# Performance work log

Hardware: AMD Instinct MI355X
Metric: run time of the kernel (lower is better)

The kernel has to match this reference:

```python
import jax, jax.numpy as jnp
import numpy as np

N, A, B, C = 256, 1024, 64, 16


def setup_inputs() -> dict:
    key = jax.random.key(0)
    k1, k2, k3 = jax.random.split(key, 3)
    x = jax.random.normal(k1, (N, A), dtype=jnp.float32)
    weight = jax.random.normal(k2, (A, B * C), dtype=jnp.float32) * 0.02
    bias = jax.random.normal(k3, (B,), dtype=jnp.float32) * 0.02
    return {"x": x, "weight": weight, "bias": bias}


def reference(x, weight, bias):
    # x: [N, A]; weight: [A, B*C]; bias: [B]
    n = x.shape[0]
    mat = (x @ weight).reshape(n, B, C)              # [N, B, C]
    # pairwise L1 over the C (kernel) axis -> [N, N, B]
    l1 = jnp.abs(mat[:, None, :, :] - mat[None, :, :, :]).sum(axis=-1)
    # exp(-L1), sum over the first (broadcast) axis as in the torch code,
    # which includes the self term exp(0)=1
    out = jnp.exp(-l1).sum(axis=0) + bias            # [N, B]
    return out
```

## Files before the change

### kernel.cpp

```cpp
#include <hip/hip_runtime.h>

#define LOG2E 1.4426950408889634f

typedef __bf16 bf16x8 __attribute__((ext_vector_type(8)));
typedef float  f32x4  __attribute__((ext_vector_type(4)));

__device__ inline unsigned short f2bf(float f){
  unsigned u = __float_as_uint(f);
  unsigned r = u + 0x7FFFu + ((u >> 16) & 1u);
  return (unsigned short)(r >> 16);
}
__device__ inline unsigned pack2(float lo, float hi){
  return (unsigned)f2bf(lo) | ((unsigned)f2bf(hi) << 16);
}

__global__ __launch_bounds__(256) void k_gemm_ks(const float* __restrict__ X,
                                                 const float* __restrict__ Wm,
                                                 float* __restrict__ P){
  __shared__ unsigned short As[64 * 72];
  __shared__ unsigned short Bs[64 * 72];
  const int m0 = blockIdx.x * 64, n0 = blockIdx.y * 64;
  const int k0 = blockIdx.z * 256;
  const int t = threadIdx.x;
  const int lane = t & 63, w = t >> 6;
  const int wrow = (w & 1) * 32, wcol = (w >> 1) * 32;
  const int r16 = lane & 15, quad = lane >> 4;

  const int ar = t >> 2, aq = t & 3;
  const int bc = t & 15, bg = t >> 4;
  const float* ap = X + (size_t)(m0 + ar) * 1024 + k0 + aq * 16;
  const float* bp = Wm + (size_t)k0 * 1024 + n0 + bc * 4;

  f32x4 acc[2][2];
  #pragma unroll
  for (int p = 0; p < 2; ++p)
    #pragma unroll
    for (int q = 0; q < 2; ++q)
      #pragma unroll
      for (int e = 0; e < 4; ++e) acc[p][q][e] = 0.f;

  float4 pa[4], pb[4];
  #pragma unroll
  for (int r = 0; r < 4; ++r) pa[r] = *(const float4*)(ap + r * 4);
  #pragma unroll
  for (int r = 0; r < 4; ++r) pb[r] = *(const float4*)(bp + (size_t)(4 * bg + r) * 1024);

  #pragma unroll
  for (int kt = 0; kt < 256; kt += 64){
    __syncthreads();
    {
      unsigned short* d = &As[ar * 72 + aq * 16];
      uint4 o;
      o.x = pack2(pa[0].x, pa[0].y); o.y = pack2(pa[0].z, pa[0].w);
      o.z = pack2(pa[1].x, pa[1].y); o.w = pack2(pa[1].z, pa[1].w);
      *(uint4*)d = o;
      o.x = pack2(pa[2].x, pa[2].y); o.y = pack2(pa[2].z, pa[2].w);
      o.z = pack2(pa[3].x, pa[3].y); o.w = pack2(pa[3].z, pa[3].w);
      *(uint4*)(d + 8) = o;
    }
    {
      #pragma unroll
      for (int e = 0; e < 4; ++e){
        const int n = bc * 4 + e;
        uint2 o;
        o.x = pack2(((const float*)&pb[0])[e], ((const float*)&pb[1])[e]);
        o.y = pack2(((const float*)&pb[2])[e], ((const float*)&pb[3])[e]);
        const int cw = (bg >> 1) ^ ((n >> 3) & 7);
        *(uint2*)(&Bs[n * 72 + cw * 8 + (bg & 1) * 4]) = o;
      }
    }
    __syncthreads();
    if (kt < 192){
      #pragma unroll
      for (int r = 0; r < 4; ++r) pa[r] = *(const float4*)(ap + kt + 64 + r * 4);
      #pragma unroll
      for (int r = 0; r < 4; ++r) pb[r] = *(const float4*)(bp + (size_t)(kt + 64 + 4 * bg + r) * 1024);
    }
    #pragma unroll
    for (int kk = 0; kk < 2; ++kk){
      const int ko = kk * 32 + quad * 8;
      bf16x8 a0 = *(const bf16x8*)(&As[(wrow      + r16) * 72 + ko]);
      bf16x8 a1 = *(const bf16x8*)(&As[(wrow + 16 + r16) * 72 + ko]);
      const int c = kk * 4 + quad;
      const int nb0 = wcol + r16, nb1 = wcol + 16 + r16;
      bf16x8 b0 = *(const bf16x8*)(&Bs[nb0 * 72 + ((c ^ ((nb0 >> 3) & 7)) * 8)]);
      bf16x8 b1 = *(const bf16x8*)(&Bs[nb1 * 72 + ((c ^ ((nb1 >> 3) & 7)) * 8)]);
      acc[0][0] = __builtin_amdgcn_mfma_f32_16x16x32_bf16(a0, b0, acc[0][0], 0, 0, 0);
      acc[0][1] = __builtin_amdgcn_mfma_f32_16x16x32_bf16(a0, b1, acc[0][1], 0, 0, 0);
      acc[1][0] = __builtin_amdgcn_mfma_f32_16x16x32_bf16(a1, b0, acc[1][0], 0, 0, 0);
      acc[1][1] = __builtin_amdgcn_mfma_f32_16x16x32_bf16(a1, b1, acc[1][1], 0, 0, 0);
    }
  }
  float* Pz = P + (size_t)blockIdx.z * 256 * 1024;
  #pragma unroll
  for (int p = 0; p < 2; ++p)
    #pragma unroll
    for (int q = 0; q < 2; ++q)
      #pragma unroll
      for (int r = 0; r < 4; ++r){
        const int row = m0 + wrow + p * 16 + quad * 4 + r;
        const int col = n0 + wcol + q * 16 + r16;
        Pz[(size_t)row * 1024 + col] = acc[p][q][r];
      }
}

__global__ __launch_bounds__(1024) void k_pair(const float* __restrict__ P,
                                               const float* __restrict__ bias,
                                               float* __restrict__ out){
  __shared__ float L[256 * 16];
  __shared__ float red[16][64];
  const int b = blockIdx.x >> 2, jc = blockIdx.x & 3;
  const int t = threadIdx.x, lane = t & 63, w = t >> 6;

  {
    const int i = t >> 2, q = t & 3;
    const float* base = P + (size_t)i * 1024 + b * 16 + q * 4;
    float4 s0 = *(const float4*)(base);
    float4 s1 = *(const float4*)(base + 256 * 1024);
    float4 s2 = *(const float4*)(base + 512 * 1024);
    float4 s3 = *(const float4*)(base + 768 * 1024);
    float4 r;
    r.x = (s0.x + s1.x) + (s2.x + s3.x);
    r.y = (s0.y + s1.y) + (s2.y + s3.y);
    r.z = (s0.z + s1.z) + (s2.z + s3.z);
    r.w = (s0.w + s1.w) + (s2.w + s3.w);
    *(float4*)(&L[i * 16 + q * 4]) = r;
  }
  __syncthreads();

  const int j = jc * 64 + lane;
  float oj[16];
  #pragma unroll
  for (int q = 0; q < 4; ++q){
    float4 v = *(const float4*)(&L[j * 16 + q * 4]);
    oj[q*4+0] = v.x; oj[q*4+1] = v.y; oj[q*4+2] = v.z; oj[q*4+3] = v.w;
  }

  float acc = 0.f;
  const int i0 = w * 16;
  #pragma unroll 4
  for (int ii = i0; ii < i0 + 16; ++ii){
    const float4* fr = (const float4*)(&L[ii * 16]);
    float4 f0 = fr[0], f1 = fr[1], f2 = fr[2], f3 = fr[3];
    float p0 = fabsf(oj[0]  - f0.x) + fabsf(oj[1]  - f0.y)
             + fabsf(oj[2]  - f0.z) + fabsf(oj[3]  - f0.w);
    float p1 = fabsf(oj[4]  - f1.x) + fabsf(oj[5]  - f1.y)
             + fabsf(oj[6]  - f1.z) + fabsf(oj[7]  - f1.w);
    float p2 = fabsf(oj[8]  - f2.x) + fabsf(oj[9]  - f2.y)
             + fabsf(oj[10] - f2.z) + fabsf(oj[11] - f2.w);
    float p3 = fabsf(oj[12] - f3.x) + fabsf(oj[13] - f3.y)
             + fabsf(oj[14] - f3.z) + fabsf(oj[15] - f3.w);
    acc += exp2f(-LOG2E * ((p0 + p1) + (p2 + p3)));
  }
  red[w][lane] = acc;
  __syncthreads();
  if (w == 0){
    float tot = 0.f;
    #pragma unroll
    for (int ww = 0; ww < 16; ++ww) tot += red[ww][lane];
    out[(size_t)j * 64 + b] = tot + bias[b];
  }
}

extern "C" void kernel_launch(void* const* d_in, const int* in_sizes, int n_in,
                              void* d_out, int out_size, void* d_ws, size_t ws_size,
                              hipStream_t stream){
  const float* x    = (const float*)d_in[0];
  const float* W    = (const float*)d_in[1];
  const float* bias = (const float*)d_in[2];
  float* out = (float*)d_out;
  float* P   = (float*)d_ws;

  k_gemm_ks<<<dim3(4, 16, 4), 256, 0, stream>>>(x, W, P);
  k_pair<<<256, 1024, 0, stream>>>(P, bias, out);
}
```

Before: 76.73 us.

## Double GEMM split-K, pad LDS strides, broadcast pair rows via readlane

The GEMM now splits K into 8 slices of 128 instead of 4 of 256, doubling the grid to 512 blocks for better CU fill. The pair kernel sums eight partial slices. LDS tiles use padded strides (76 and 20) in place of the XOR swizzle. The pair loop broadcasts the i-row values across the wavefront with readlane instead of reading them from LDS, and the log2e scale is folded into the operands. The cost is twice the partial-sum traffic to and from the workspace, plus scalar readlane pressure in the inner loop.

```diff
diff --git a/kernel.cpp b/kernel.cpp
--- a/kernel.cpp
+++ b/kernel.cpp
@@ -4,6 +4,9 @@
 
 typedef __bf16 bf16x8 __attribute__((ext_vector_type(8)));
 typedef float  f32x4  __attribute__((ext_vector_type(4)));
+
+#define TSTR 76
+#define LSTR 20
 
 __device__ inline unsigned short f2bf(float f){
   unsigned u = __float_as_uint(f);
@@ -17,10 +20,10 @@
 __global__ __launch_bounds__(256) void k_gemm_ks(const float* __restrict__ X,
                                                  const float* __restrict__ Wm,
                                                  float* __restrict__ P){
-  __shared__ unsigned short As[64 * 72];
-  __shared__ unsigned short Bs[64 * 72];
+  __shared__ unsigned short As[64 * TSTR];
+  __shared__ unsigned short Bs[64 * TSTR];
   const int m0 = blockIdx.x * 64, n0 = blockIdx.y * 64;
-  const int k0 = blockIdx.z * 256;
+  const int k0 = blockIdx.z * 128;
   const int t = threadIdx.x;
   const int lane = t & 63, w = t >> 6;
   const int wrow = (w & 1) * 32, wcol = (w >> 1) * 32;
@@ -46,10 +49,10 @@
   for (int r = 0; r < 4; ++r) pb[r] = *(const float4*)(bp + (size_t)(4 * bg + r) * 1024);
 
   #pragma unroll
-  for (int kt = 0; kt < 256; kt += 64){
+  for (int kt = 0; kt < 128; kt += 64){
     __syncthreads();
     {
-      unsigned short* d = &As[ar * 72 + aq * 16];
+      unsigned short* d = &As[ar * TSTR + aq * 16];
       uint4 o;
       o.x = pack2(pa[0].x, pa[0].y); o.y = pack2(pa[0].z, pa[0].w);
       o.z = pack2(pa[1].x, pa[1].y); o.w = pack2(pa[1].z, pa[1].w);
@@ -65,26 +68,23 @@
         uint2 o;
         o.x = pack2(((const float*)&pb[0])[e], ((const float*)&pb[1])[e]);
         o.y = pack2(((const float*)&pb[2])[e], ((const float*)&pb[3])[e]);
-        const int cw = (bg >> 1) ^ ((n >> 3) & 7);
-        *(uint2*)(&Bs[n * 72 + cw * 8 + (bg & 1) * 4]) = o;
+        *(uint2*)(&Bs[n * TSTR + bg * 4]) = o;
       }
     }
     __syncthreads();
-    if (kt < 192){
+    if (kt < 64){
       #pragma unroll
-      for (int r = 0; r < 4; ++r) pa[r] = *(const float4*)(ap + kt + 64 + r * 4);
+      for (int r = 0; r < 4; ++r) pa[r] = *(const float4*)(ap + 64 + r * 4);
       #pragma unroll
-      for (int r = 0; r < 4; ++r) pb[r] = *(const float4*)(bp + (size_t)(kt + 64 + 4 * bg + r) * 1024);
+      for (int r = 0; r < 4; ++r) pb[r] = *(const float4*)(bp + (size_t)(64 + 4 * bg + r) * 1024);
     }
     #pragma unroll
     for (int kk = 0; kk < 2; ++kk){
       const int ko = kk * 32 + quad * 8;
-      bf16x8 a0 = *(const bf16x8*)(&As[(wrow      + r16) * 72 + ko]);
-      bf16x8 a1 = *(const bf16x8*)(&As[(wrow + 16 + r16) * 72 + ko]);
-      const int c = kk * 4 + quad;
-      const int nb0 = wcol + r16, nb1 = wcol + 16 + r16;
-      bf16x8 b0 = *(const bf16x8*)(&Bs[nb0 * 72 + ((c ^ ((nb0 >> 3) & 7)) * 8)]);
-      bf16x8 b1 = *(const bf16x8*)(&Bs[nb1 * 72 + ((c ^ ((nb1 >> 3) & 7)) * 8)]);
+      bf16x8 a0 = *(const bf16x8*)(&As[(wrow      + r16) * TSTR + ko]);
+      bf16x8 a1 = *(const bf16x8*)(&As[(wrow + 16 + r16) * TSTR + ko]);
+      bf16x8 b0 = *(const bf16x8*)(&Bs[(wcol      + r16) * TSTR + ko]);
+      bf16x8 b1 = *(const bf16x8*)(&Bs[(wcol + 16 + r16) * TSTR + ko]);
       acc[0][0] = __builtin_amdgcn_mfma_f32_16x16x32_bf16(a0, b0, acc[0][0], 0, 0, 0);
       acc[0][1] = __builtin_amdgcn_mfma_f32_16x16x32_bf16(a0, b1, acc[0][1], 0, 0, 0);
       acc[1][0] = __builtin_amdgcn_mfma_f32_16x16x32_bf16(a1, b0, acc[1][0], 0, 0, 0);
@@ -107,7 +107,7 @@
 __global__ __launch_bounds__(1024) void k_pair(const float* __restrict__ P,
                                                const float* __restrict__ bias,
                                                float* __restrict__ out){
-  __shared__ float L[256 * 16];
+  __shared__ float L[256 * LSTR];
   __shared__ float red[16][64];
   const int b = blockIdx.x >> 2, jc = blockIdx.x & 3;
   const int t = threadIdx.x, lane = t & 63, w = t >> 6;
@@ -116,15 +116,19 @@
     const int i = t >> 2, q = t & 3;
     const float* base = P + (size_t)i * 1024 + b * 16 + q * 4;
     float4 s0 = *(const float4*)(base);
-    float4 s1 = *(const float4*)(base + 256 * 1024);
-    float4 s2 = *(const float4*)(base + 512 * 1024);
-    float4 s3 = *(const float4*)(base + 768 * 1024);
+    float4 s1 = *(const float4*)(base + 1 * 262144);
+    float4 s2 = *(const float4*)(base + 2 * 262144);
+    float4 s3 = *(const float4*)(base + 3 * 262144);
+    float4 s4 = *(const float4*)(base + 4 * 262144);
+    float4 s5 = *(const float4*)(base + 5 * 262144);
+    float4 s6 = *(const float4*)(base + 6 * 262144);
+    float4 s7 = *(const float4*)(base + 7 * 262144);
     float4 r;
-    r.x = (s0.x + s1.x) + (s2.x + s3.x);
-    r.y = (s0.y + s1.y) + (s2.y + s3.y);
-    r.z = (s0.z + s1.z) + (s2.z + s3.z);
-    r.w = (s0.w + s1.w) + (s2.w + s3.w);
-    *(float4*)(&L[i * 16 + q * 4]) = r;
+    r.x = ((s0.x + s1.x) + (s2.x + s3.x)) + ((s4.x + s5.x) + (s6.x + s7.x));
+    r.y = ((s0.y + s1.y) + (s2.y + s3.y)) + ((s4.y + s5.y) + (s6.y + s7.y));
+    r.z = ((s0.z + s1.z) + (s2.z + s3.z)) + ((s4.z + s5.z) + (s6.z + s7.z));
+    r.w = ((s0.w + s1.w) + (s2.w + s3.w)) + ((s4.w + s5.w) + (s6.w + s7.w));
+    *(float4*)(&L[i * LSTR + q * 4]) = r;
   }
   __syncthreads();
 
@@ -132,27 +136,39 @@
   float oj[16];
   #pragma unroll
   for (int q = 0; q < 4; ++q){
-    float4 v = *(const float4*)(&L[j * 16 + q * 4]);
-    oj[q*4+0] = v.x; oj[q*4+1] = v.y; oj[q*4+2] = v.z; oj[q*4+3] = v.w;
+    float4 v = *(const float4*)(&L[j * LSTR + q * 4]);
+    oj[q*4+0] = v.x * LOG2E; oj[q*4+1] = v.y * LOG2E;
+    oj[q*4+2] = v.z * LOG2E; oj[q*4+3] = v.w * LOG2E;
   }
+  float4 vi = *(const float4*)(&L[(w * 16 + (lane >> 2)) * LSTR + (lane & 3) * 4]);
+  const int i0 = __float_as_int(vi.x * LOG2E);
+  const int i1 = __float_as_int(vi.y * LOG2E);
+  const int i2 = __float_as_int(vi.z * LOG2E);
+  const int i3 = __float_as_int(vi.w * LOG2E);
 
-  float acc = 0.f;
-  const int i0 = w * 16;
+  float accs = 0.f;
   #pragma unroll 4
-  for (int ii = i0; ii < i0 + 16; ++ii){
-    const float4* fr = (const float4*)(&L[ii * 16]);
-    float4 f0 = fr[0], f1 = fr[1], f2 = fr[2], f3 = fr[3];
-    float p0 = fabsf(oj[0]  - f0.x) + fabsf(oj[1]  - f0.y)
-             + fabsf(oj[2]  - f0.z) + fabsf(oj[3]  - f0.w);
-    float p1 = fabsf(oj[4]  - f1.x) + fabsf(oj[5]  - f1.y)
-             + fabsf(oj[6]  - f1.z) + fabsf(oj[7]  - f1.w);
-    float p2 = fabsf(oj[8]  - f2.x) + fabsf(oj[9]  - f2.y)
-             + fabsf(oj[10] - f2.z) + fabsf(oj[11] - f2.w);
-    float p3 = fabsf(oj[12] - f3.x) + fabsf(oj[13] - f3.y)
-             + fabsf(oj[14] - f3.z) + fabsf(oj[15] - f3.w);
-    acc += exp2f(-LOG2E * ((p0 + p1) + (p2 + p3)));
+  for (int ii = 0; ii < 16; ++ii){
+    const int sl = ii * 4;
+    float p0 = fabsf(oj[0]  - __int_as_float(__builtin_amdgcn_readlane(i0, sl)))
+             + fabsf(oj[1]  - __int_as_float(__builtin_amdgcn_readlane(i1, sl)))
+             + fabsf(oj[2]  - __int_as_float(__builtin_amdgcn_readlane(i2, sl)))
+             + fabsf(oj[3]  - __int_as_float(__builtin_amdgcn_readlane(i3, sl)));
+    float p1 = fabsf(oj[4]  - __int_as_float(__builtin_amdgcn_readlane(i0, sl + 1)))
+             + fabsf(oj[5]  - __int_as_float(__builtin_amdgcn_readlane(i1, sl + 1)))
+             + fabsf(oj[6]  - __int_as_float(__builtin_amdgcn_readlane(i2, sl + 1)))
+             + fabsf(oj[7]  - __int_as_float(__builtin_amdgcn_readlane(i3, sl + 1)));
+    float p2 = fabsf(oj[8]  - __int_as_float(__builtin_amdgcn_readlane(i0, sl + 2)))
+             + fabsf(oj[9]  - __int_as_float(__builtin_amdgcn_readlane(i1, sl + 2)))
+             + fabsf(oj[10] - __int_as_float(__builtin_amdgcn_readlane(i2, sl + 2)))
+             + fabsf(oj[11] - __int_as_float(__builtin_amdgcn_readlane(i3, sl + 2)));
+    float p3 = fabsf(oj[12] - __int_as_float(__builtin_amdgcn_readlane(i0, sl + 3)))
+             + fabsf(oj[13] - __int_as_float(__builtin_amdgcn_readlane(i1, sl + 3)))
+             + fabsf(oj[14] - __int_as_float(__builtin_amdgcn_readlane(i2, sl + 3)))
+             + fabsf(oj[15] - __int_as_float(__builtin_amdgcn_readlane(i3, sl + 3)));
+    accs += exp2f(-((p0 + p1) + (p2 + p3)));
   }
-  red[w][lane] = acc;
+  red[w][lane] = accs;
   __syncthreads();
   if (w == 0){
     float tot = 0.f;
@@ -171,6 +187,6 @@
   float* out = (float*)d_out;
   float* P   = (float*)d_ws;
 
-  k_gemm_ks<<<dim3(4, 16, 4), 256, 0, stream>>>(x, W, P);
+  k_gemm_ks<<<dim3(4, 16, 8), 256, 0, stream>>>(x, W, P);
   k_pair<<<256, 1024, 0, stream>>>(P, bias, out);
 }
```

New measurement: 84.10 us. 9.6% more time.
